# Kernel optimization log

Hardware: AMD Instinct MI355X
Metric: run time of the kernel (lower is better)

Reference implementation:

```python
import jax, jax.numpy as jnp
import numpy as np

EPS = 1e-12  # torch F.normalize eps

def _l2norm(v, axis):
    n = jnp.sqrt(jnp.sum(v * v, axis=axis, keepdims=True))
    return v / jnp.maximum(n, EPS)

def setup_inputs() -> dict:
    key = jax.random.key(0)
    k1, k2, k3 = jax.random.split(key, 3)
    N, D, H, W, K = 32, 512, 56, 56, 64
    x = jax.random.normal(k1, (N, D, H, W), dtype=jnp.float32)
    conv_w = jax.random.normal(k2, (K, D), dtype=jnp.float32) * 0.05
    centroids = jax.random.uniform(k3, (K, D), dtype=jnp.float32)
    return {"x": x, "conv_w": conv_w, "centroids": centroids}

def reference(x, conv_w, centroids):
    N, D, H, W = x.shape
    K = centroids.shape[0]
    # descriptor-wise L2 normalization over channel dim
    x = _l2norm(x, axis=1)
    x_flat = x.reshape(N, D, H * W)                      # (N, D, P)
    # 1x1 conv == per-pixel linear map: (K,D) x (N,D,P) -> (N,K,P)
    logits = jnp.einsum('kd,ndp->nkp', conv_w, x_flat)
    soft_assign = jax.nn.softmax(logits, axis=1)         # softmax over clusters
    # vlad[n,k,:] = sum_p a[n,k,p] * (x[n,:,p] - c[k,:])
    #            = (a @ x^T)[n,k,:] - (sum_p a[n,k,p]) * c[k,:]
    agg = jnp.einsum('nkp,ndp->nkd', soft_assign, x_flat)           # (N, K, D)
    a_sum = jnp.sum(soft_assign, axis=2)                            # (N, K)
    vlad = agg - a_sum[:, :, None] * centroids[None, :, :]
    vlad = _l2norm(vlad, axis=2)        # intra-normalization per cluster
    vlad = vlad.reshape(N, K * D)
    vlad = _l2norm(vlad, axis=1)        # global L2 normalization
    return vlad
```

## Files before the change

### kernel.cpp

```cpp
#include <hip/hip_runtime.h>
#include <hip/hip_bf16.h>

typedef unsigned short u16;
typedef unsigned int u32;
typedef __bf16 bf16x8 __attribute__((ext_vector_type(8)));
typedef float f32x4 __attribute__((ext_vector_type(4)));

#define N_ 32
#define D_ 512
#define P_ 3136
#define K_ 64
#define TILES_P 49
#define NDP (D_ * P_)


__device__ __forceinline__ u16 f2bf(float f) {
  u32 u = __float_as_uint(f);
  return (u16)((u + 0x7fffu + ((u >> 16) & 1u)) >> 16);
}
__device__ __forceinline__ u32 pack2(float a, float b) {
  return (u32)f2bf(a) | ((u32)f2bf(b) << 16);
}

__global__ __launch_bounds__(256) void kw_kernel(const float* __restrict__ w,
                                                 u16* __restrict__ wbf) {
  int i = blockIdx.x * 256 + threadIdx.x;
  float4 v = ((const float4*)w)[i];
  ((uint2*)wbf)[i] = make_uint2(pack2(v.x, v.y), pack2(v.z, v.w));
}

__global__ __launch_bounds__(256) void k1_kernel(const float* __restrict__ x,
                                                 const u16* __restrict__ wbf,
                                                 u16* __restrict__ a_ws,
                                                 float* __restrict__ a_sum) {
  __shared__ float a_stage[64][65];
  __shared__ float invn_s[64];

  const int t = threadIdx.x;
  const int bid = blockIdx.x;
  const int n = bid / TILES_P;
  const int tile = bid - n * TILES_P;
  const int p0 = tile * 64;
  const int lane = t & 63;
  const int w = t >> 6;
  const int c = lane & 15;
  const int q = lane >> 4;
  const int rp = w * 16 + c;

  const float* xl = x + (size_t)n * NDP + p0 + rp + (size_t)(q * 8) * P_;

  f32x4 acc[4];
#pragma unroll
  for (int m = 0; m < 4; ++m) acc[m] = (f32x4){0.f, 0.f, 0.f, 0.f};
  float sumsq = 0.f;

  float v[8];
#pragma unroll
  for (int j = 0; j < 8; ++j) v[j] = xl[j * P_];

  for (int s = 0; s < 16; ++s) {
    float vn[8];
    if (s < 15) {
      const float* xs = xl + (size_t)((s + 1) * 32) * P_;
#pragma unroll
      for (int j = 0; j < 8; ++j) vn[j] = xs[j * P_];
    }
    bf16x8 bfrag;
#pragma unroll
    for (int j = 0; j < 8; ++j) {
      sumsq += v[j] * v[j];
      bfrag[j] = (__bf16)v[j];
    }
#pragma unroll
    for (int m = 0; m < 4; ++m) {
      bf16x8 afrag = ((const bf16x8*)wbf)[(m * 16 + c) * 64 + s * 4 + q];
      acc[m] = __builtin_amdgcn_mfma_f32_16x16x32_bf16(afrag, bfrag, acc[m], 0, 0, 0);
    }
    if (s < 15) {
#pragma unroll
      for (int j = 0; j < 8; ++j) v[j] = vn[j];
    }
  }

  sumsq += __shfl_xor(sumsq, 16);
  sumsq += __shfl_xor(sumsq, 32);
  const float inv_p = 1.f / fmaxf(sqrtf(sumsq), 1e-12f);
  if (q == 0) invn_s[rp] = inv_p;

  float sc[4][4];
  float lmax = -3.0e38f;
#pragma unroll
  for (int m = 0; m < 4; ++m)
#pragma unroll
    for (int r = 0; r < 4; ++r) {
      float val = acc[m][r] * inv_p;
      sc[m][r] = val;
      lmax = fmaxf(lmax, val);
    }
  lmax = fmaxf(lmax, __shfl_xor(lmax, 16));
  lmax = fmaxf(lmax, __shfl_xor(lmax, 32));
  float lsum = 0.f;
#pragma unroll
  for (int m = 0; m < 4; ++m)
#pragma unroll
    for (int r = 0; r < 4; ++r) {
      float e = __expf(sc[m][r] - lmax);
      sc[m][r] = e;
      lsum += e;
    }
  lsum += __shfl_xor(lsum, 16);
  lsum += __shfl_xor(lsum, 32);
  const float rs = 1.f / lsum;
#pragma unroll
  for (int m = 0; m < 4; ++m)
#pragma unroll
    for (int r = 0; r < 4; ++r)
      a_stage[m * 16 + q * 4 + r][rp] = sc[m][r] * rs;
  __syncthreads();

  {
    const int k = t >> 2, pc = t & 3;
    float ssum = 0.f;
    u32 u[8];
#pragma unroll
    for (int jj = 0; jj < 8; ++jj) {
      int p = pc * 16 + jj * 2;
      float a0 = a_stage[k][p], a1 = a_stage[k][p + 1];
      ssum += a0 + a1;
      u[jj] = (u32)f2bf(a0 * invn_s[p]) | ((u32)f2bf(a1 * invn_s[p + 1]) << 16);
    }
    u16* dst = a_ws + (size_t)n * (K_ * P_) + k * P_ + p0 + pc * 16;
    ((uint4*)dst)[0] = make_uint4(u[0], u[1], u[2], u[3]);
    ((uint4*)dst)[1] = make_uint4(u[4], u[5], u[6], u[7]);
    ssum += __shfl_xor(ssum, 1);
    ssum += __shfl_xor(ssum, 2);
    if ((t & 3) == 0) atomicAdd(&a_sum[n * 64 + k], ssum);
  }
}

__global__ __launch_bounds__(256) void k2_kernel(const float* __restrict__ x,
                                                 const u16* __restrict__ a_ws,
                                                 float* __restrict__ agg) {
  const int bid = blockIdx.x;
  const int n = bid / 56;
  const int rem = bid - n * 56;
  const int dblk = rem / 7;
  const int pp = rem - dblk * 7;
  const int t = threadIdx.x;
  const int lane = t & 63, w = t >> 6;
  const int c = lane & 15, q = lane >> 4;
  const int d0 = dblk * 64 + w * 16;

  f32x4 acc[4];
#pragma unroll
  for (int m = 0; m < 4; ++m) acc[m] = (f32x4){0.f, 0.f, 0.f, 0.f};

  const bf16x8* arow = (const bf16x8*)(a_ws + (size_t)n * (K_ * P_));
  const float4* xf = (const float4*)(x + ((size_t)n * D_ + d0 + c) * P_);
  const int it0 = pp * 14, it1 = it0 + 14;

  float4 b0 = xf[it0 * 8 + q * 2];
  float4 b1 = xf[it0 * 8 + q * 2 + 1];
  bf16x8 af0 = arow[(0 * 16 + c) * 392 + it0 * 4 + q];
  bf16x8 af1 = arow[(1 * 16 + c) * 392 + it0 * 4 + q];
  bf16x8 af2 = arow[(2 * 16 + c) * 392 + it0 * 4 + q];
  bf16x8 af3 = arow[(3 * 16 + c) * 392 + it0 * 4 + q];

#pragma unroll
  for (int it = it0; it < it1; ++it) {
    float4 nb0, nb1;
    bf16x8 nf0, nf1, nf2, nf3;
    if (it + 1 < it1) {
      nb0 = xf[(it + 1) * 8 + q * 2];
      nb1 = xf[(it + 1) * 8 + q * 2 + 1];
      nf0 = arow[(0 * 16 + c) * 392 + (it + 1) * 4 + q];
      nf1 = arow[(1 * 16 + c) * 392 + (it + 1) * 4 + q];
      nf2 = arow[(2 * 16 + c) * 392 + (it + 1) * 4 + q];
      nf3 = arow[(3 * 16 + c) * 392 + (it + 1) * 4 + q];
    }
    bf16x8 bfrag;
    bfrag[0] = (__bf16)b0.x; bfrag[1] = (__bf16)b0.y;
    bfrag[2] = (__bf16)b0.z; bfrag[3] = (__bf16)b0.w;
    bfrag[4] = (__bf16)b1.x; bfrag[5] = (__bf16)b1.y;
    bfrag[6] = (__bf16)b1.z; bfrag[7] = (__bf16)b1.w;
    acc[0] = __builtin_amdgcn_mfma_f32_16x16x32_bf16(af0, bfrag, acc[0], 0, 0, 0);
    acc[1] = __builtin_amdgcn_mfma_f32_16x16x32_bf16(af1, bfrag, acc[1], 0, 0, 0);
    acc[2] = __builtin_amdgcn_mfma_f32_16x16x32_bf16(af2, bfrag, acc[2], 0, 0, 0);
    acc[3] = __builtin_amdgcn_mfma_f32_16x16x32_bf16(af3, bfrag, acc[3], 0, 0, 0);
    if (it + 1 < it1) {
      b0 = nb0; b1 = nb1; af0 = nf0; af1 = nf1; af2 = nf2; af3 = nf3;
    }
  }
  float* ob = agg + ((size_t)pp * 32 + n) * (K_ * D_);
#pragma unroll
  for (int m = 0; m < 4; ++m)
#pragma unroll
    for (int r = 0; r < 4; ++r)
      ob[(m * 16 + q * 4 + r) * D_ + d0 + c] = acc[m][r];
}

__global__ __launch_bounds__(64) void k3a_kernel(const float* __restrict__ agg,
                                                 const float* __restrict__ a_sum,
                                                 const float* __restrict__ cent,
                                                 float* __restrict__ out,
                                                 float* __restrict__ rowsq) {
  const int b = blockIdx.x;
  const int n = b >> 6, k = b & 63;
  const int t = threadIdx.x;
  const float* ab = agg + ((size_t)n * 64 + k) * 512 + t * 8;
  float v[8];
#pragma unroll
  for (int j = 0; j < 8; ++j) v[j] = 0.f;
#pragma unroll
  for (int pp = 0; pp < 7; ++pp) {
    const float4* p4 = (const float4*)(ab + (size_t)pp * 32 * (K_ * D_));
    float4 r0 = p4[0], r1 = p4[1];
    v[0] += r0.x; v[1] += r0.y; v[2] += r0.z; v[3] += r0.w;
    v[4] += r1.x; v[5] += r1.y; v[6] += r1.z; v[7] += r1.w;
  }
  const float asum = a_sum[b];
  const float4* c4 = (const float4*)(cent + k * 512 + t * 8);
  float4 c0 = c4[0], c1 = c4[1];
  v[0] -= asum * c0.x; v[1] -= asum * c0.y; v[2] -= asum * c0.z; v[3] -= asum * c0.w;
  v[4] -= asum * c1.x; v[5] -= asum * c1.y; v[6] -= asum * c1.z; v[7] -= asum * c1.w;
  float ss = 0.f;
#pragma unroll
  for (int j = 0; j < 8; ++j) ss += v[j] * v[j];
  ss += __shfl_xor(ss, 1);  ss += __shfl_xor(ss, 2);  ss += __shfl_xor(ss, 4);
  ss += __shfl_xor(ss, 8);  ss += __shfl_xor(ss, 16); ss += __shfl_xor(ss, 32);
  float4* o4 = (float4*)(out + (size_t)n * 32768 + k * 512 + t * 8);
  o4[0] = make_float4(v[0], v[1], v[2], v[3]);
  o4[1] = make_float4(v[4], v[5], v[6], v[7]);
  if (t == 0) rowsq[b] = ss;
}

__global__ __launch_bounds__(256) void k3b_kernel(const float* __restrict__ rowsq,
                                                  float* __restrict__ out) {
  __shared__ float invr_s[64];
  __shared__ float gi_s;
  const int n = blockIdx.x >> 3;
  const int seg = blockIdx.x & 7;
  const int t = threadIdx.x;
  if (t < 64) {
    float r = rowsq[n * 64 + t];
    float ri = 1.f / fmaxf(sqrtf(r), 1e-12f);
    invr_s[t] = ri;
    float g = r * ri * ri;
    g += __shfl_xor(g, 1); g += __shfl_xor(g, 2); g += __shfl_xor(g, 4);
    g += __shfl_xor(g, 8); g += __shfl_xor(g, 16); g += __shfl_xor(g, 32);
    if (t == 0) gi_s = 1.f / fmaxf(sqrtf(g), 1e-12f);
  }
  __syncthreads();
  const int e0 = seg * 4096 + t * 16;
  const float sc = invr_s[e0 >> 9] * gi_s;
  float4* o4 = (float4*)(out + (size_t)n * 32768 + e0);
#pragma unroll
  for (int i = 0; i < 4; ++i) {
    float4 vv = o4[i];
    vv.x *= sc; vv.y *= sc; vv.z *= sc; vv.w *= sc;
    o4[i] = vv;
  }
}

extern "C" void kernel_launch(void* const* d_in, const int* in_sizes, int n_in,
                              void* d_out, int out_size, void* d_ws, size_t ws_size,
                              hipStream_t stream) {
  (void)in_sizes; (void)n_in; (void)out_size; (void)ws_size;
  const float* x    = (const float*)d_in[0];
  const float* cw   = (const float*)d_in[1];
  const float* cent = (const float*)d_in[2];
  float* out = (float*)d_out;
  char* ws = (char*)d_ws;
  u16*   wbf   = (u16*)(ws);
  u16*   a_ws  = (u16*)(ws + 65536);
  float* a_sum = (float*)(ws + 12910592);
  float* agg   = (float*)(ws + 12918784);
  float* rowsq = (float*)(ws + 42278912);

  hipMemsetAsync(a_sum, 0, 64 * 32 * sizeof(float), stream);
  kw_kernel<<<32, 256, 0, stream>>>(cw, wbf);
  k1_kernel<<<32 * TILES_P, 256, 0, stream>>>(x, wbf, a_ws, a_sum);
  k2_kernel<<<1792, 256, 0, stream>>>(x, a_ws, agg);
  k3a_kernel<<<2048, 64, 0, stream>>>(agg, a_sum, cent, out, rowsq);
  k3b_kernel<<<256, 256, 0, stream>>>(rowsq, out);
}
```

Before: 393.9 us.

## Stage x tile through swizzled LDS in k1, deepen k2 prefetch, remap k2 blocks

k1 now loads the x tile with coalesced float4 reads, converts it to bf16 and writes it into a 64KB XOR-swizzled LDS buffer. The MFMA B fragments are then read from LDS, replacing strided scalar global loads along the channel dimension. The per-pixel sum of squares is reduced through shared memory, and the weight fragments are double-buffered. k2 prefetches two iterations ahead and remaps block IDs so blocks on the same XCD share batch data. The cost is 64KB of LDS per block, which likely limits occupancy, plus an extra barrier.

```diff
diff --git a/kernel.cpp b/kernel.cpp
--- a/kernel.cpp
+++ b/kernel.cpp
@@ -33,59 +33,89 @@
                                                  const u16* __restrict__ wbf,
                                                  u16* __restrict__ a_ws,
                                                  float* __restrict__ a_sum) {
-  __shared__ float a_stage[64][65];
+  __shared__ __align__(16) char xbuf[65536];
+  __shared__ float red[4][64];
   __shared__ float invn_s[64];
+  u16* X = (u16*)xbuf;
+  float (*a_stage)[65] = (float (*)[65])xbuf;
 
   const int t = threadIdx.x;
+  const int lane = t & 63;
+  const int w = t >> 6;
+  const int c = lane & 15;
+  const int q = lane >> 4;
   const int bid = blockIdx.x;
   const int n = bid / TILES_P;
   const int tile = bid - n * TILES_P;
   const int p0 = tile * 64;
-  const int lane = t & 63;
-  const int w = t >> 6;
-  const int c = lane & 15;
-  const int q = lane >> 4;
   const int rp = w * 16 + c;
 
-  const float* xl = x + (size_t)n * NDP + p0 + rp + (size_t)(q * 8) * P_;
-
-  f32x4 acc[4];
-#pragma unroll
-  for (int m = 0; m < 4; ++m) acc[m] = (f32x4){0.f, 0.f, 0.f, 0.f};
-  float sumsq = 0.f;
-
-  float v[8];
-#pragma unroll
-  for (int j = 0; j < 8; ++j) v[j] = xl[j * P_];
-
-  for (int s = 0; s < 16; ++s) {
-    float vn[8];
-    if (s < 15) {
-      const float* xs = xl + (size_t)((s + 1) * 32) * P_;
-#pragma unroll
-      for (int j = 0; j < 8; ++j) vn[j] = xs[j * P_];
-    }
-    bf16x8 bfrag;
-#pragma unroll
-    for (int j = 0; j < 8; ++j) {
-      sumsq += v[j] * v[j];
-      bfrag[j] = (__bf16)v[j];
-    }
-#pragma unroll
-    for (int m = 0; m < 4; ++m) {
-      bf16x8 afrag = ((const bf16x8*)wbf)[(m * 16 + c) * 64 + s * 4 + q];
-      acc[m] = __builtin_amdgcn_mfma_f32_16x16x32_bf16(afrag, bfrag, acc[m], 0, 0, 0);
-    }
-    if (s < 15) {
-#pragma unroll
-      for (int j = 0; j < 8; ++j) v[j] = vn[j];
-    }
-  }
-
-  sumsq += __shfl_xor(sumsq, 16);
-  sumsq += __shfl_xor(sumsq, 32);
+  const float* xg = x + (size_t)n * NDP + p0 + c * 4;
+  float La[8][4][4];
+#pragma unroll
+  for (int g = 0; g < 8; ++g) {
+    const int dr = g * 64 + w * 16 + q * 4;
+#pragma unroll
+    for (int i = 0; i < 4; ++i) {
+      float4 v4 = *(const float4*)(xg + (size_t)(dr + i) * P_);
+      La[g][i][0] = v4.x; La[g][i][1] = v4.y; La[g][i][2] = v4.z; La[g][i][3] = v4.w;
+    }
+  }
+  float ss[4] = {0.f, 0.f, 0.f, 0.f};
+#pragma unroll
+  for (int g = 0; g < 8; ++g) {
+    const int dr = g * 64 + w * 16 + q * 4;
+    const int chunk = dr >> 3;
+    const int sub = (q & 1) * 8;
+#pragma unroll
+    for (int j = 0; j < 4; ++j) {
+      float v0 = La[g][0][j], v1 = La[g][1][j], v2 = La[g][2][j], v3 = La[g][3][j];
+      ss[j] += v0 * v0 + v1 * v1 + v2 * v2 + v3 * v3;
+      const int p = c * 4 + j;
+      const int byte = p * 1024 + (((chunk ^ (p & 7)) << 4) | sub);
+      *(uint2*)(xbuf + byte) = make_uint2(pack2(v0, v1), pack2(v2, v3));
+    }
+  }
+#pragma unroll
+  for (int j = 0; j < 4; ++j) {
+    ss[j] += __shfl_xor(ss[j], 16);
+    ss[j] += __shfl_xor(ss[j], 32);
+  }
+  if (q == 0) {
+#pragma unroll
+    for (int j = 0; j < 4; ++j) red[w][c * 4 + j] = ss[j];
+  }
+  __syncthreads();
+
+  const float sumsq = red[0][rp] + red[1][rp] + red[2][rp] + red[3][rp];
   const float inv_p = 1.f / fmaxf(sqrtf(sumsq), 1e-12f);
   if (q == 0) invn_s[rp] = inv_p;
+
+  f32x4 acc[4];
+#pragma unroll
+  for (int m = 0; m < 4; ++m) acc[m] = (f32x4){0.f, 0.f, 0.f, 0.f};
+  const int ds_base = rp * 1024;
+  const int rmask = rp & 7;
+  bf16x8 af[4];
+#pragma unroll
+  for (int m = 0; m < 4; ++m) af[m] = ((const bf16x8*)wbf)[(m * 16 + c) * 64 + q];
+#pragma unroll
+  for (int s = 0; s < 16; ++s) {
+    bf16x8 afn[4];
+    if (s < 15) {
+#pragma unroll
+      for (int m = 0; m < 4; ++m)
+        afn[m] = ((const bf16x8*)wbf)[(m * 16 + c) * 64 + (s + 1) * 4 + q];
+    }
+    bf16x8 bfrag = *(const bf16x8*)(xbuf + ds_base + (((s * 4 + q) ^ rmask) << 4));
+#pragma unroll
+    for (int m = 0; m < 4; ++m)
+      acc[m] = __builtin_amdgcn_mfma_f32_16x16x32_bf16(af[m], bfrag, acc[m], 0, 0, 0);
+    if (s < 15) {
+#pragma unroll
+      for (int m = 0; m < 4; ++m) af[m] = afn[m];
+    }
+  }
 
   float sc[4][4];
   float lmax = -3.0e38f;
@@ -111,6 +141,8 @@
   lsum += __shfl_xor(lsum, 16);
   lsum += __shfl_xor(lsum, 32);
   const float rs = 1.f / lsum;
+
+  __syncthreads();
 #pragma unroll
   for (int m = 0; m < 4; ++m)
 #pragma unroll
@@ -141,7 +173,8 @@
 __global__ __launch_bounds__(256) void k2_kernel(const float* __restrict__ x,
                                                  const u16* __restrict__ a_ws,
                                                  float* __restrict__ agg) {
-  const int bid = blockIdx.x;
+  int bid = blockIdx.x;
+  bid = (bid & 7) * 224 + (bid >> 3);
   const int n = bid / 56;
   const int rem = bid - n * 56;
   const int dblk = rem / 7;
@@ -157,39 +190,39 @@
 
   const bf16x8* arow = (const bf16x8*)(a_ws + (size_t)n * (K_ * P_));
   const float4* xf = (const float4*)(x + ((size_t)n * D_ + d0 + c) * P_);
-  const int it0 = pp * 14, it1 = it0 + 14;
-
-  float4 b0 = xf[it0 * 8 + q * 2];
-  float4 b1 = xf[it0 * 8 + q * 2 + 1];
-  bf16x8 af0 = arow[(0 * 16 + c) * 392 + it0 * 4 + q];
-  bf16x8 af1 = arow[(1 * 16 + c) * 392 + it0 * 4 + q];
-  bf16x8 af2 = arow[(2 * 16 + c) * 392 + it0 * 4 + q];
-  bf16x8 af3 = arow[(3 * 16 + c) * 392 + it0 * 4 + q];
-
-#pragma unroll
-  for (int it = it0; it < it1; ++it) {
-    float4 nb0, nb1;
-    bf16x8 nf0, nf1, nf2, nf3;
-    if (it + 1 < it1) {
-      nb0 = xf[(it + 1) * 8 + q * 2];
-      nb1 = xf[(it + 1) * 8 + q * 2 + 1];
-      nf0 = arow[(0 * 16 + c) * 392 + (it + 1) * 4 + q];
-      nf1 = arow[(1 * 16 + c) * 392 + (it + 1) * 4 + q];
-      nf2 = arow[(2 * 16 + c) * 392 + (it + 1) * 4 + q];
-      nf3 = arow[(3 * 16 + c) * 392 + (it + 1) * 4 + q];
+  const int it0 = pp * 14;
+
+  float4 pb[2][2];
+  bf16x8 pa[2][4];
+#pragma unroll
+  for (int k2 = 0; k2 < 2; ++k2) {
+    pb[k2][0] = xf[(it0 + k2) * 8 + q * 2];
+    pb[k2][1] = xf[(it0 + k2) * 8 + q * 2 + 1];
+#pragma unroll
+    for (int m = 0; m < 4; ++m)
+      pa[k2][m] = arow[(m * 16 + c) * 392 + (it0 + k2) * 4 + q];
+  }
+#pragma unroll
+  for (int ii = 0; ii < 14; ++ii) {
+    const int cur = ii & 1;
+    float4 b0 = pb[cur][0], b1 = pb[cur][1];
+    bf16x8 a0_ = pa[cur][0], a1_ = pa[cur][1], a2_ = pa[cur][2], a3_ = pa[cur][3];
+    if (ii < 12) {
+      pb[cur][0] = xf[(it0 + ii + 2) * 8 + q * 2];
+      pb[cur][1] = xf[(it0 + ii + 2) * 8 + q * 2 + 1];
+#pragma unroll
+      for (int m = 0; m < 4; ++m)
+        pa[cur][m] = arow[(m * 16 + c) * 392 + (it0 + ii + 2) * 4 + q];
     }
     bf16x8 bfrag;
     bfrag[0] = (__bf16)b0.x; bfrag[1] = (__bf16)b0.y;
     bfrag[2] = (__bf16)b0.z; bfrag[3] = (__bf16)b0.w;
     bfrag[4] = (__bf16)b1.x; bfrag[5] = (__bf16)b1.y;
     bfrag[6] = (__bf16)b1.z; bfrag[7] = (__bf16)b1.w;
-    acc[0] = __builtin_amdgcn_mfma_f32_16x16x32_bf16(af0, bfrag, acc[0], 0, 0, 0);
-    acc[1] = __builtin_amdgcn_mfma_f32_16x16x32_bf16(af1, bfrag, acc[1], 0, 0, 0);
-    acc[2] = __builtin_amdgcn_mfma_f32_16x16x32_bf16(af2, bfrag, acc[2], 0, 0, 0);
-    acc[3] = __builtin_amdgcn_mfma_f32_16x16x32_bf16(af3, bfrag, acc[3], 0, 0, 0);
-    if (it + 1 < it1) {
-      b0 = nb0; b1 = nb1; af0 = nf0; af1 = nf1; af2 = nf2; af3 = nf3;
-    }
+    acc[0] = __builtin_amdgcn_mfma_f32_16x16x32_bf16(a0_, bfrag, acc[0], 0, 0, 0);
+    acc[1] = __builtin_amdgcn_mfma_f32_16x16x32_bf16(a1_, bfrag, acc[1], 0, 0, 0);
+    acc[2] = __builtin_amdgcn_mfma_f32_16x16x32_bf16(a2_, bfrag, acc[2], 0, 0, 0);
+    acc[3] = __builtin_amdgcn_mfma_f32_16x16x32_bf16(a3_, bfrag, acc[3], 0, 0, 0);
   }
   float* ob = agg + ((size_t)pp * 32 + n) * (K_ * D_);
 #pragma unroll
@@ -223,15 +256,15 @@
   float4 c0 = c4[0], c1 = c4[1];
   v[0] -= asum * c0.x; v[1] -= asum * c0.y; v[2] -= asum * c0.z; v[3] -= asum * c0.w;
   v[4] -= asum * c1.x; v[5] -= asum * c1.y; v[6] -= asum * c1.z; v[7] -= asum * c1.w;
-  float ss = 0.f;
-#pragma unroll
-  for (int j = 0; j < 8; ++j) ss += v[j] * v[j];
-  ss += __shfl_xor(ss, 1);  ss += __shfl_xor(ss, 2);  ss += __shfl_xor(ss, 4);
-  ss += __shfl_xor(ss, 8);  ss += __shfl_xor(ss, 16); ss += __shfl_xor(ss, 32);
+  float ssq = 0.f;
+#pragma unroll
+  for (int j = 0; j < 8; ++j) ssq += v[j] * v[j];
+  ssq += __shfl_xor(ssq, 1);  ssq += __shfl_xor(ssq, 2);  ssq += __shfl_xor(ssq, 4);
+  ssq += __shfl_xor(ssq, 8);  ssq += __shfl_xor(ssq, 16); ssq += __shfl_xor(ssq, 32);
   float4* o4 = (float4*)(out + (size_t)n * 32768 + k * 512 + t * 8);
   o4[0] = make_float4(v[0], v[1], v[2], v[3]);
   o4[1] = make_float4(v[4], v[5], v[6], v[7]);
-  if (t == 0) rowsq[b] = ss;
+  if (t == 0) rowsq[b] = ssq;
 }
 
 __global__ __launch_bounds__(256) void k3b_kernel(const float* __restrict__ rowsq,
```

New measurement: 403.2 us. 1.02x slower.

## Pre-convert x to bf16 and transpose it for the logits GEMM

Applied to the files above, without the earlier changes.

Adds a pass that casts the whole input to bf16. A second pass transposes it to pixel-major layout and precomputes per-pixel squared norms. The logits kernel then loads contiguous bf16x8 fragments with two-deep prefetch, and the aggregation kernel reads bf16 x instead of fp32. The aggregation grid ordering is remapped, and the residual kernel packs four clusters per 256-thread block. In exchange, the extra cast and transpose passes add substantial memory traffic. The transpose uses scalar strided 16-bit loads, and the norms are now computed from bf16-rounded values.

```diff
diff --git a/kernel.cpp b/kernel.cpp
--- a/kernel.cpp
+++ b/kernel.cpp
@@ -29,13 +29,61 @@
   ((uint2*)wbf)[i] = make_uint2(pack2(v.x, v.y), pack2(v.z, v.w));
 }
 
-__global__ __launch_bounds__(256) void k1_kernel(const float* __restrict__ x,
+__global__ __launch_bounds__(256) void tbf_kernel(const float* __restrict__ x,
+                                                  u16* __restrict__ xbf) {
+  const int nf4 = (N_ * NDP) / 4;
+  for (int i = blockIdx.x * 256 + threadIdx.x; i < nf4; i += 2048 * 256) {
+    float4 v = ((const float4*)x)[i];
+    ((uint2*)xbf)[i] = make_uint2(pack2(v.x, v.y), pack2(v.z, v.w));
+  }
+}
+
+__global__ __launch_bounds__(256) void tt_kernel(const u16* __restrict__ xbf,
+                                                 u16* __restrict__ xt,
+                                                 float* __restrict__ psum) {
+  const int bid = blockIdx.x;
+  const int n = bid / TILES_P;
+  const int tile = bid - n * TILES_P;
+  const int p0 = tile * 64;
+  const int t = threadIdx.x;
+  const int lane = t & 63;
+  const int w = t >> 6;
+  const int c = lane & 15;
+  const int q = lane >> 4;
+  const int gpx = p0 + w * 16 + c;
+
+  const u16* src = xbf + (size_t)n * NDP + gpx;
+  u16* dst = xt + ((size_t)n * P_ + gpx) * D_;
+  float s0 = 0.f, s1 = 0.f;
+#pragma unroll
+  for (int it = 0; it < 16; ++it) {
+    const u16* sp = src + (size_t)(it * 32 + q * 8) * P_;
+    u32 u[4];
+#pragma unroll
+    for (int j = 0; j < 4; ++j) {
+      u32 lo = sp[(size_t)(2 * j) * P_];
+      u32 hi = sp[(size_t)(2 * j + 1) * P_];
+      u[j] = lo | (hi << 16);
+      float f0 = __uint_as_float(lo << 16);
+      float f1 = __uint_as_float(hi << 16);
+      s0 += f0 * f0;
+      s1 += f1 * f1;
+    }
+    *(uint4*)(dst + it * 32 + q * 8) = make_uint4(u[0], u[1], u[2], u[3]);
+  }
+  float ssq = s0 + s1;
+  ssq += __shfl_xor(ssq, 16);
+  ssq += __shfl_xor(ssq, 32);
+  if (q == 0) psum[n * P_ + gpx] = ssq;
+}
+
+__global__ __launch_bounds__(256) void k1_kernel(const u16* __restrict__ xt,
                                                  const u16* __restrict__ wbf,
+                                                 const float* __restrict__ psum,
                                                  u16* __restrict__ a_ws,
                                                  float* __restrict__ a_sum) {
   __shared__ float a_stage[64][65];
   __shared__ float invn_s[64];
-
   const int t = threadIdx.x;
   const int bid = blockIdx.x;
   const int n = bid / TILES_P;
@@ -47,45 +95,42 @@
   const int q = lane >> 4;
   const int rp = w * 16 + c;
 
-  const float* xl = x + (size_t)n * NDP + p0 + rp + (size_t)(q * 8) * P_;
+  if (t < 64)
+    invn_s[t] = 1.f / fmaxf(sqrtf(psum[n * P_ + p0 + t]), 1e-12f);
+  const float inv_p = 1.f / fmaxf(sqrtf(psum[n * P_ + p0 + rp]), 1e-12f);
+
+  const bf16x8* brow = (const bf16x8*)(xt + ((size_t)n * P_ + p0 + rp) * D_);
+  const bf16x8* wrow = (const bf16x8*)wbf;
 
   f32x4 acc[4];
 #pragma unroll
   for (int m = 0; m < 4; ++m) acc[m] = (f32x4){0.f, 0.f, 0.f, 0.f};
-  float sumsq = 0.f;
-
-  float v[8];
-#pragma unroll
-  for (int j = 0; j < 8; ++j) v[j] = xl[j * P_];
-
+
+  bf16x8 pb[2];
+  bf16x8 pa[2][4];
+  pb[0] = brow[q];
+  pb[1] = brow[4 + q];
+#pragma unroll
+  for (int m = 0; m < 4; ++m) {
+    pa[0][m] = wrow[(m * 16 + c) * 64 + q];
+    pa[1][m] = wrow[(m * 16 + c) * 64 + 4 + q];
+  }
+#pragma unroll
   for (int s = 0; s < 16; ++s) {
-    float vn[8];
-    if (s < 15) {
-      const float* xs = xl + (size_t)((s + 1) * 32) * P_;
-#pragma unroll
-      for (int j = 0; j < 8; ++j) vn[j] = xs[j * P_];
-    }
-    bf16x8 bfrag;
-#pragma unroll
-    for (int j = 0; j < 8; ++j) {
-      sumsq += v[j] * v[j];
-      bfrag[j] = (__bf16)v[j];
-    }
-#pragma unroll
-    for (int m = 0; m < 4; ++m) {
-      bf16x8 afrag = ((const bf16x8*)wbf)[(m * 16 + c) * 64 + s * 4 + q];
-      acc[m] = __builtin_amdgcn_mfma_f32_16x16x32_bf16(afrag, bfrag, acc[m], 0, 0, 0);
-    }
-    if (s < 15) {
-#pragma unroll
-      for (int j = 0; j < 8; ++j) v[j] = vn[j];
-    }
-  }
-
-  sumsq += __shfl_xor(sumsq, 16);
-  sumsq += __shfl_xor(sumsq, 32);
-  const float inv_p = 1.f / fmaxf(sqrtf(sumsq), 1e-12f);
-  if (q == 0) invn_s[rp] = inv_p;
+    const int cur = s & 1;
+    bf16x8 bfr = pb[cur];
+    bf16x8 a0 = pa[cur][0], a1 = pa[cur][1], a2 = pa[cur][2], a3 = pa[cur][3];
+    if (s < 14) {
+      pb[cur] = brow[(s + 2) * 4 + q];
+#pragma unroll
+      for (int m = 0; m < 4; ++m)
+        pa[cur][m] = wrow[(m * 16 + c) * 64 + (s + 2) * 4 + q];
+    }
+    acc[0] = __builtin_amdgcn_mfma_f32_16x16x32_bf16(a0, bfr, acc[0], 0, 0, 0);
+    acc[1] = __builtin_amdgcn_mfma_f32_16x16x32_bf16(a1, bfr, acc[1], 0, 0, 0);
+    acc[2] = __builtin_amdgcn_mfma_f32_16x16x32_bf16(a2, bfr, acc[2], 0, 0, 0);
+    acc[3] = __builtin_amdgcn_mfma_f32_16x16x32_bf16(a3, bfr, acc[3], 0, 0, 0);
+  }
 
   float sc[4][4];
   float lmax = -3.0e38f;
@@ -138,14 +183,14 @@
   }
 }
 
-__global__ __launch_bounds__(256) void k2_kernel(const float* __restrict__ x,
+__global__ __launch_bounds__(256) void k2_kernel(const u16* __restrict__ xbf,
                                                  const u16* __restrict__ a_ws,
                                                  float* __restrict__ agg) {
-  const int bid = blockIdx.x;
-  const int n = bid / 56;
-  const int rem = bid - n * 56;
-  const int dblk = rem / 7;
-  const int pp = rem - dblk * 7;
+  const int b = blockIdx.x;
+  const int dblk = (b >> 3) & 7;
+  const int npp = (b >> 6) * 8 + (b & 7);
+  const int n = npp / 7;
+  const int pp = npp - n * 7;
   const int t = threadIdx.x;
   const int lane = t & 63, w = t >> 6;
   const int c = lane & 15, q = lane >> 4;
@@ -155,41 +200,33 @@
 #pragma unroll
   for (int m = 0; m < 4; ++m) acc[m] = (f32x4){0.f, 0.f, 0.f, 0.f};
 
-  const bf16x8* arow = (const bf16x8*)(a_ws + (size_t)n * (K_ * P_));
-  const float4* xf = (const float4*)(x + ((size_t)n * D_ + d0 + c) * P_);
-  const int it0 = pp * 14, it1 = it0 + 14;
-
-  float4 b0 = xf[it0 * 8 + q * 2];
-  float4 b1 = xf[it0 * 8 + q * 2 + 1];
-  bf16x8 af0 = arow[(0 * 16 + c) * 392 + it0 * 4 + q];
-  bf16x8 af1 = arow[(1 * 16 + c) * 392 + it0 * 4 + q];
-  bf16x8 af2 = arow[(2 * 16 + c) * 392 + it0 * 4 + q];
-  bf16x8 af3 = arow[(3 * 16 + c) * 392 + it0 * 4 + q];
-
-#pragma unroll
-  for (int it = it0; it < it1; ++it) {
-    float4 nb0, nb1;
-    bf16x8 nf0, nf1, nf2, nf3;
-    if (it + 1 < it1) {
-      nb0 = xf[(it + 1) * 8 + q * 2];
-      nb1 = xf[(it + 1) * 8 + q * 2 + 1];
-      nf0 = arow[(0 * 16 + c) * 392 + (it + 1) * 4 + q];
-      nf1 = arow[(1 * 16 + c) * 392 + (it + 1) * 4 + q];
-      nf2 = arow[(2 * 16 + c) * 392 + (it + 1) * 4 + q];
-      nf3 = arow[(3 * 16 + c) * 392 + (it + 1) * 4 + q];
-    }
-    bf16x8 bfrag;
-    bfrag[0] = (__bf16)b0.x; bfrag[1] = (__bf16)b0.y;
-    bfrag[2] = (__bf16)b0.z; bfrag[3] = (__bf16)b0.w;
-    bfrag[4] = (__bf16)b1.x; bfrag[5] = (__bf16)b1.y;
-    bfrag[6] = (__bf16)b1.z; bfrag[7] = (__bf16)b1.w;
-    acc[0] = __builtin_amdgcn_mfma_f32_16x16x32_bf16(af0, bfrag, acc[0], 0, 0, 0);
-    acc[1] = __builtin_amdgcn_mfma_f32_16x16x32_bf16(af1, bfrag, acc[1], 0, 0, 0);
-    acc[2] = __builtin_amdgcn_mfma_f32_16x16x32_bf16(af2, bfrag, acc[2], 0, 0, 0);
-    acc[3] = __builtin_amdgcn_mfma_f32_16x16x32_bf16(af3, bfrag, acc[3], 0, 0, 0);
-    if (it + 1 < it1) {
-      b0 = nb0; b1 = nb1; af0 = nf0; af1 = nf1; af2 = nf2; af3 = nf3;
-    }
+  const u16* ab = a_ws + (size_t)n * (K_ * P_) + pp * 448 + q * 8;
+  const u16* xb = xbf + ((size_t)n * D_ + d0 + c) * P_ + pp * 448 + q * 8;
+
+  bf16x8 pb[2];
+  bf16x8 pa[2][4];
+#pragma unroll
+  for (int k2 = 0; k2 < 2; ++k2) {
+    pb[k2] = *(const bf16x8*)(xb + k2 * 32);
+#pragma unroll
+    for (int m = 0; m < 4; ++m)
+      pa[k2][m] = *(const bf16x8*)(ab + (size_t)(m * 16 + c) * P_ + k2 * 32);
+  }
+#pragma unroll
+  for (int it = 0; it < 14; ++it) {
+    const int cur = it & 1;
+    bf16x8 bfr = pb[cur];
+    bf16x8 a0 = pa[cur][0], a1 = pa[cur][1], a2 = pa[cur][2], a3 = pa[cur][3];
+    if (it < 12) {
+      pb[cur] = *(const bf16x8*)(xb + (it + 2) * 32);
+#pragma unroll
+      for (int m = 0; m < 4; ++m)
+        pa[cur][m] = *(const bf16x8*)(ab + (size_t)(m * 16 + c) * P_ + (it + 2) * 32);
+    }
+    acc[0] = __builtin_amdgcn_mfma_f32_16x16x32_bf16(a0, bfr, acc[0], 0, 0, 0);
+    acc[1] = __builtin_amdgcn_mfma_f32_16x16x32_bf16(a1, bfr, acc[1], 0, 0, 0);
+    acc[2] = __builtin_amdgcn_mfma_f32_16x16x32_bf16(a2, bfr, acc[2], 0, 0, 0);
+    acc[3] = __builtin_amdgcn_mfma_f32_16x16x32_bf16(a3, bfr, acc[3], 0, 0, 0);
   }
   float* ob = agg + ((size_t)pp * 32 + n) * (K_ * D_);
 #pragma unroll
@@ -199,15 +236,17 @@
       ob[(m * 16 + q * 4 + r) * D_ + d0 + c] = acc[m][r];
 }
 
-__global__ __launch_bounds__(64) void k3a_kernel(const float* __restrict__ agg,
-                                                 const float* __restrict__ a_sum,
-                                                 const float* __restrict__ cent,
-                                                 float* __restrict__ out,
-                                                 float* __restrict__ rowsq) {
+__global__ __launch_bounds__(256) void k3a_kernel(const float* __restrict__ agg,
+                                                  const float* __restrict__ a_sum,
+                                                  const float* __restrict__ cent,
+                                                  float* __restrict__ out,
+                                                  float* __restrict__ rowsq) {
   const int b = blockIdx.x;
-  const int n = b >> 6, k = b & 63;
-  const int t = threadIdx.x;
-  const float* ab = agg + ((size_t)n * 64 + k) * 512 + t * 8;
+  const int n = b >> 4, kg = b & 15;
+  const int t = threadIdx.x;
+  const int lane = t & 63, w = t >> 6;
+  const int k = kg * 4 + w;
+  const float* ab = agg + ((size_t)n * 64 + k) * 512 + lane * 8;
   float v[8];
 #pragma unroll
   for (int j = 0; j < 8; ++j) v[j] = 0.f;
@@ -218,20 +257,20 @@
     v[0] += r0.x; v[1] += r0.y; v[2] += r0.z; v[3] += r0.w;
     v[4] += r1.x; v[5] += r1.y; v[6] += r1.z; v[7] += r1.w;
   }
-  const float asum = a_sum[b];
-  const float4* c4 = (const float4*)(cent + k * 512 + t * 8);
+  const float asum = a_sum[n * 64 + k];
+  const float4* c4 = (const float4*)(cent + k * 512 + lane * 8);
   float4 c0 = c4[0], c1 = c4[1];
   v[0] -= asum * c0.x; v[1] -= asum * c0.y; v[2] -= asum * c0.z; v[3] -= asum * c0.w;
   v[4] -= asum * c1.x; v[5] -= asum * c1.y; v[6] -= asum * c1.z; v[7] -= asum * c1.w;
-  float ss = 0.f;
-#pragma unroll
-  for (int j = 0; j < 8; ++j) ss += v[j] * v[j];
-  ss += __shfl_xor(ss, 1);  ss += __shfl_xor(ss, 2);  ss += __shfl_xor(ss, 4);
-  ss += __shfl_xor(ss, 8);  ss += __shfl_xor(ss, 16); ss += __shfl_xor(ss, 32);
-  float4* o4 = (float4*)(out + (size_t)n * 32768 + k * 512 + t * 8);
+  float ssq = 0.f;
+#pragma unroll
+  for (int j = 0; j < 8; ++j) ssq += v[j] * v[j];
+  ssq += __shfl_xor(ssq, 1);  ssq += __shfl_xor(ssq, 2);  ssq += __shfl_xor(ssq, 4);
+  ssq += __shfl_xor(ssq, 8);  ssq += __shfl_xor(ssq, 16); ssq += __shfl_xor(ssq, 32);
+  float4* o4 = (float4*)(out + (size_t)n * 32768 + k * 512 + lane * 8);
   o4[0] = make_float4(v[0], v[1], v[2], v[3]);
   o4[1] = make_float4(v[4], v[5], v[6], v[7]);
-  if (t == 0) rowsq[b] = ss;
+  if (lane == 0) rowsq[n * 64 + k] = ssq;
 }
 
 __global__ __launch_bounds__(256) void k3b_kernel(const float* __restrict__ rowsq,
@@ -276,11 +315,16 @@
   float* a_sum = (float*)(ws + 12910592);
   float* agg   = (float*)(ws + 12918784);
   float* rowsq = (float*)(ws + 42278912);
+  u16*   xbf   = (u16*)(ws + 42287104);
+  u16*   x_t   = (u16*)(ws + 145047552);
+  float* psum  = (float*)(ws + 247808000);
 
   hipMemsetAsync(a_sum, 0, 64 * 32 * sizeof(float), stream);
   kw_kernel<<<32, 256, 0, stream>>>(cw, wbf);
-  k1_kernel<<<32 * TILES_P, 256, 0, stream>>>(x, wbf, a_ws, a_sum);
-  k2_kernel<<<1792, 256, 0, stream>>>(x, a_ws, agg);
-  k3a_kernel<<<2048, 64, 0, stream>>>(agg, a_sum, cent, out, rowsq);
+  tbf_kernel<<<2048, 256, 0, stream>>>(x, xbf);
+  tt_kernel<<<32 * TILES_P, 256, 0, stream>>>(xbf, x_t, psum);
+  k1_kernel<<<32 * TILES_P, 256, 0, stream>>>(x_t, wbf, psum, a_ws, a_sum);
+  k2_kernel<<<1792, 256, 0, stream>>>(xbf, a_ws, agg);
+  k3a_kernel<<<512, 256, 0, stream>>>(agg, a_sum, cent, out, rowsq);
   k3b_kernel<<<256, 256, 0, stream>>>(rowsq, out);
 }
```

Result: slower. 491.7 us (+24.8%).

## Fuse soft-assignment and aggregation into one LDS-staged kernel reading x once

Applied to the files above, without the earlier changes.

Merges the logits/softmax kernel and the aggregation GEMM into a single kernel. Each block owns one batch item and a range of pixel tiles, stages a 512x64 fp32 x tile into 128KB of LDS with a swizzle via global_load_lds, and computes both GEMMs from that shared copy. The aim is to read x from HBM once instead of twice and to skip the bf16 assignment round-trip through global memory. In exchange only 256 blocks of one wave-group each run, with 128 fp32 accumulators per thread and no overlap between loads and compute, so latency hiding and occupancy may suffer.

```diff
diff --git a/kernel.cpp b/kernel.cpp
--- a/kernel.cpp
+++ b/kernel.cpp
@@ -10,7 +10,6 @@
 #define D_ 512
 #define P_ 3136
 #define K_ 64
-#define TILES_P 49
 #define NDP (D_ * P_)
 
 
@@ -29,209 +28,232 @@
   ((uint2*)wbf)[i] = make_uint2(pack2(v.x, v.y), pack2(v.z, v.w));
 }
 
-__global__ __launch_bounds__(256) void k1_kernel(const float* __restrict__ x,
-                                                 const u16* __restrict__ wbf,
-                                                 u16* __restrict__ a_ws,
-                                                 float* __restrict__ a_sum) {
+__global__ __launch_bounds__(256, 1) void f_kernel(const float* __restrict__ x,
+                                                   const u16* __restrict__ wbf,
+                                                   float* __restrict__ agg,
+                                                   float* __restrict__ a_sum) {
+  __shared__ __align__(16) char xbuf[131072];
   __shared__ float a_stage[64][65];
   __shared__ float invn_s[64];
+  __shared__ __align__(16) char a_bf[8192];
 
   const int t = threadIdx.x;
-  const int bid = blockIdx.x;
-  const int n = bid / TILES_P;
-  const int tile = bid - n * TILES_P;
-  const int p0 = tile * 64;
   const int lane = t & 63;
   const int w = t >> 6;
   const int c = lane & 15;
   const int q = lane >> 4;
+  const int b = blockIdx.x;
+  const int n = b >> 3;
+  const int s = b & 7;
+  const int tile0 = (s == 0) ? 0 : 7 + (s - 1) * 6;
+  const int ntl = (s == 0) ? 7 : 6;
   const int rp = w * 16 + c;
-
-  const float* xl = x + (size_t)n * NDP + p0 + rp + (size_t)(q * 8) * P_;
-
-  f32x4 acc[4];
-#pragma unroll
-  for (int m = 0; m < 4; ++m) acc[m] = (f32x4){0.f, 0.f, 0.f, 0.f};
-  float sumsq = 0.f;
-
-  float v[8];
-#pragma unroll
-  for (int j = 0; j < 8; ++j) v[j] = xl[j * P_];
-
-  for (int s = 0; s < 16; ++s) {
-    float vn[8];
-    if (s < 15) {
-      const float* xs = xl + (size_t)((s + 1) * 32) * P_;
-#pragma unroll
-      for (int j = 0; j < 8; ++j) vn[j] = xs[j * P_];
-    }
-    bf16x8 bfrag;
-#pragma unroll
-    for (int j = 0; j < 8; ++j) {
-      sumsq += v[j] * v[j];
-      bfrag[j] = (__bf16)v[j];
-    }
+  const int rpc = rp >> 2;
+  const int rpo = (rp & 3) * 4;
+  const int c7 = c & 7;
+
+  const bf16x8* wrow = (const bf16x8*)wbf;
+  const char* xgb = (const char*)(x + (size_t)n * NDP);
+
+  f32x4 acc2[4][8];
+#pragma unroll
+  for (int m = 0; m < 4; ++m)
+#pragma unroll
+    for (int i = 0; i < 8; ++i) acc2[m][i] = (f32x4){0.f, 0.f, 0.f, 0.f};
+  float ssum_acc = 0.f;
+
+  for (int tt = 0; tt < ntl; ++tt) {
+    const int p0 = (tile0 + tt) * 64;
+
+#pragma unroll
+    for (int i = 0; i < 32; ++i) {
+      const int d = w * 128 + i * 4 + q;
+      const char* src = xgb + ((size_t)d * P_ + p0) * 4 + ((c ^ (d & 7)) << 4);
+      __builtin_amdgcn_global_load_lds(
+          (const __attribute__((address_space(1))) void*)src,
+          (__attribute__((address_space(3))) void*)(xbuf + w * 32768 + i * 1024),
+          16, 0, 0);
+    }
+    __syncthreads();
+
+    f32x4 acc[4];
+#pragma unroll
+    for (int m = 0; m < 4; ++m) acc[m] = (f32x4){0.f, 0.f, 0.f, 0.f};
+    float sumsq = 0.f;
+    bf16x8 pa[2][4];
 #pragma unroll
     for (int m = 0; m < 4; ++m) {
-      bf16x8 afrag = ((const bf16x8*)wbf)[(m * 16 + c) * 64 + s * 4 + q];
-      acc[m] = __builtin_amdgcn_mfma_f32_16x16x32_bf16(afrag, bfrag, acc[m], 0, 0, 0);
-    }
-    if (s < 15) {
-#pragma unroll
-      for (int j = 0; j < 8; ++j) v[j] = vn[j];
-    }
+      pa[0][m] = wrow[(m * 16 + c) * 64 + q];
+      pa[1][m] = wrow[(m * 16 + c) * 64 + 4 + q];
+    }
+    float vc[8];
+#pragma unroll
+    for (int j = 0; j < 8; ++j)
+      vc[j] = *(const float*)(xbuf + ((q * 8 + j) << 8) + ((rpc ^ j) << 4) + rpo);
+#pragma unroll
+    for (int st = 0; st < 16; ++st) {
+      float vn[8];
+      if (st < 15) {
+#pragma unroll
+        for (int j = 0; j < 8; ++j)
+          vn[j] = *(const float*)(xbuf + (((st + 1) * 32 + q * 8 + j) << 8) +
+                                  ((rpc ^ j) << 4) + rpo);
+      }
+      bf16x8 bfr;
+#pragma unroll
+      for (int j = 0; j < 8; ++j) {
+        sumsq += vc[j] * vc[j];
+        bfr[j] = (__bf16)vc[j];
+      }
+      bf16x8 nf[4];
+      if (st < 14) {
+#pragma unroll
+        for (int m = 0; m < 4; ++m)
+          nf[m] = wrow[(m * 16 + c) * 64 + (st + 2) * 4 + q];
+      }
+#pragma unroll
+      for (int m = 0; m < 4; ++m)
+        acc[m] = __builtin_amdgcn_mfma_f32_16x16x32_bf16(pa[st & 1][m], bfr, acc[m], 0, 0, 0);
+      if (st < 14) {
+#pragma unroll
+        for (int m = 0; m < 4; ++m) pa[st & 1][m] = nf[m];
+      }
+      if (st < 15) {
+#pragma unroll
+        for (int j = 0; j < 8; ++j) vc[j] = vn[j];
+      }
+    }
+
+    sumsq += __shfl_xor(sumsq, 16);
+    sumsq += __shfl_xor(sumsq, 32);
+    const float inv_p = 1.f / fmaxf(sqrtf(sumsq), 1e-12f);
+    if (q == 0) invn_s[rp] = inv_p;
+
+    float sc[4][4];
+    float lmax = -3.0e38f;
+#pragma unroll
+    for (int m = 0; m < 4; ++m)
+#pragma unroll
+      for (int r = 0; r < 4; ++r) {
+        float val = acc[m][r] * inv_p;
+        sc[m][r] = val;
+        lmax = fmaxf(lmax, val);
+      }
+    lmax = fmaxf(lmax, __shfl_xor(lmax, 16));
+    lmax = fmaxf(lmax, __shfl_xor(lmax, 32));
+    float lsum = 0.f;
+#pragma unroll
+    for (int m = 0; m < 4; ++m)
+#pragma unroll
+      for (int r = 0; r < 4; ++r) {
+        float e = __expf(sc[m][r] - lmax);
+        sc[m][r] = e;
+        lsum += e;
+      }
+    lsum += __shfl_xor(lsum, 16);
+    lsum += __shfl_xor(lsum, 32);
+    const float rs = 1.f / lsum;
+#pragma unroll
+    for (int m = 0; m < 4; ++m)
+#pragma unroll
+      for (int r = 0; r < 4; ++r)
+        a_stage[m * 16 + q * 4 + r][rp] = sc[m][r] * rs;
+    __syncthreads();
+
+    {
+      const int k = t >> 2, pc4 = t & 3;
+      float ssum = 0.f;
+      u32 u[8];
+#pragma unroll
+      for (int jj = 0; jj < 8; ++jj) {
+        int p = pc4 * 16 + jj * 2;
+        float a0 = a_stage[k][p], a1 = a_stage[k][p + 1];
+        ssum += a0 + a1;
+        u[jj] = (u32)f2bf(a0 * invn_s[p]) | ((u32)f2bf(a1 * invn_s[p + 1]) << 16);
+      }
+      *(uint4*)(a_bf + k * 128 + (((pc4 * 2) ^ (k & 7)) << 4)) =
+          make_uint4(u[0], u[1], u[2], u[3]);
+      *(uint4*)(a_bf + k * 128 + (((pc4 * 2 + 1) ^ (k & 7)) << 4)) =
+          make_uint4(u[4], u[5], u[6], u[7]);
+      ssum_acc += ssum;
+    }
+    __syncthreads();
+
+#pragma unroll
+    for (int st = 0; st < 2; ++st) {
+      bf16x8 afr[4];
+#pragma unroll
+      for (int m = 0; m < 4; ++m)
+        afr[m] = *(const bf16x8*)(a_bf + (m * 16 + c) * 128 +
+                                  (((st * 4 + q) ^ c7) << 4));
+      const int pc0 = st * 8 + q * 2;
+#pragma unroll
+      for (int nt = 0; nt < 8; ++nt) {
+        const int d = w * 128 + nt * 16 + c;
+        f32x4 b0 = *(const f32x4*)(xbuf + (d << 8) + ((pc0 ^ c7) << 4));
+        f32x4 b1 = *(const f32x4*)(xbuf + (d << 8) + (((pc0 + 1) ^ c7) << 4));
+        bf16x8 bfr;
+#pragma unroll
+        for (int i4 = 0; i4 < 4; ++i4) {
+          bfr[i4] = (__bf16)b0[i4];
+          bfr[4 + i4] = (__bf16)b1[i4];
+        }
+#pragma unroll
+        for (int m = 0; m < 4; ++m)
+          acc2[m][nt] = __builtin_amdgcn_mfma_f32_16x16x32_bf16(afr[m], bfr, acc2[m][nt], 0, 0, 0);
+      }
+    }
+    __syncthreads();
   }
 
-  sumsq += __shfl_xor(sumsq, 16);
-  sumsq += __shfl_xor(sumsq, 32);
-  const float inv_p = 1.f / fmaxf(sqrtf(sumsq), 1e-12f);
-  if (q == 0) invn_s[rp] = inv_p;
-
-  float sc[4][4];
-  float lmax = -3.0e38f;
+  float* ob = agg + ((size_t)s * 32 + n) * (K_ * D_);
 #pragma unroll
   for (int m = 0; m < 4; ++m)
 #pragma unroll
-    for (int r = 0; r < 4; ++r) {
-      float val = acc[m][r] * inv_p;
-      sc[m][r] = val;
-      lmax = fmaxf(lmax, val);
-    }
-  lmax = fmaxf(lmax, __shfl_xor(lmax, 16));
-  lmax = fmaxf(lmax, __shfl_xor(lmax, 32));
-  float lsum = 0.f;
-#pragma unroll
-  for (int m = 0; m < 4; ++m)
-#pragma unroll
-    for (int r = 0; r < 4; ++r) {
-      float e = __expf(sc[m][r] - lmax);
-      sc[m][r] = e;
-      lsum += e;
-    }
-  lsum += __shfl_xor(lsum, 16);
-  lsum += __shfl_xor(lsum, 32);
-  const float rs = 1.f / lsum;
-#pragma unroll
-  for (int m = 0; m < 4; ++m)
-#pragma unroll
-    for (int r = 0; r < 4; ++r)
-      a_stage[m * 16 + q * 4 + r][rp] = sc[m][r] * rs;
-  __syncthreads();
-
-  {
-    const int k = t >> 2, pc = t & 3;
-    float ssum = 0.f;
-    u32 u[8];
-#pragma unroll
-    for (int jj = 0; jj < 8; ++jj) {
-      int p = pc * 16 + jj * 2;
-      float a0 = a_stage[k][p], a1 = a_stage[k][p + 1];
-      ssum += a0 + a1;
-      u[jj] = (u32)f2bf(a0 * invn_s[p]) | ((u32)f2bf(a1 * invn_s[p + 1]) << 16);
-    }
-    u16* dst = a_ws + (size_t)n * (K_ * P_) + k * P_ + p0 + pc * 16;
-    ((uint4*)dst)[0] = make_uint4(u[0], u[1], u[2], u[3]);
-    ((uint4*)dst)[1] = make_uint4(u[4], u[5], u[6], u[7]);
-    ssum += __shfl_xor(ssum, 1);
-    ssum += __shfl_xor(ssum, 2);
-    if ((t & 3) == 0) atomicAdd(&a_sum[n * 64 + k], ssum);
-  }
-}
-
-__global__ __launch_bounds__(256) void k2_kernel(const float* __restrict__ x,
-                                                 const u16* __restrict__ a_ws,
-                                                 float* __restrict__ agg) {
-  const int bid = blockIdx.x;
-  const int n = bid / 56;
-  const int rem = bid - n * 56;
-  const int dblk = rem / 7;
-  const int pp = rem - dblk * 7;
+    for (int nt = 0; nt < 8; ++nt)
+#pragma unroll
+      for (int r = 0; r < 4; ++r)
+        ob[(m * 16 + q * 4 + r) * D_ + w * 128 + nt * 16 + c] = acc2[m][nt][r];
+  ssum_acc += __shfl_xor(ssum_acc, 1);
+  ssum_acc += __shfl_xor(ssum_acc, 2);
+  if ((t & 3) == 0) atomicAdd(&a_sum[n * 64 + (t >> 2)], ssum_acc);
+}
+
+__global__ __launch_bounds__(256) void k3a_kernel(const float* __restrict__ agg,
+                                                  const float* __restrict__ a_sum,
+                                                  const float* __restrict__ cent,
+                                                  float* __restrict__ out,
+                                                  float* __restrict__ rowsq) {
+  const int b = blockIdx.x;
+  const int n = b >> 4, kg = b & 15;
   const int t = threadIdx.x;
   const int lane = t & 63, w = t >> 6;
-  const int c = lane & 15, q = lane >> 4;
-  const int d0 = dblk * 64 + w * 16;
-
-  f32x4 acc[4];
-#pragma unroll
-  for (int m = 0; m < 4; ++m) acc[m] = (f32x4){0.f, 0.f, 0.f, 0.f};
-
-  const bf16x8* arow = (const bf16x8*)(a_ws + (size_t)n * (K_ * P_));
-  const float4* xf = (const float4*)(x + ((size_t)n * D_ + d0 + c) * P_);
-  const int it0 = pp * 14, it1 = it0 + 14;
-
-  float4 b0 = xf[it0 * 8 + q * 2];
-  float4 b1 = xf[it0 * 8 + q * 2 + 1];
-  bf16x8 af0 = arow[(0 * 16 + c) * 392 + it0 * 4 + q];
-  bf16x8 af1 = arow[(1 * 16 + c) * 392 + it0 * 4 + q];
-  bf16x8 af2 = arow[(2 * 16 + c) * 392 + it0 * 4 + q];
-  bf16x8 af3 = arow[(3 * 16 + c) * 392 + it0 * 4 + q];
-
-#pragma unroll
-  for (int it = it0; it < it1; ++it) {
-    float4 nb0, nb1;
-    bf16x8 nf0, nf1, nf2, nf3;
-    if (it + 1 < it1) {
-      nb0 = xf[(it + 1) * 8 + q * 2];
-      nb1 = xf[(it + 1) * 8 + q * 2 + 1];
-      nf0 = arow[(0 * 16 + c) * 392 + (it + 1) * 4 + q];
-      nf1 = arow[(1 * 16 + c) * 392 + (it + 1) * 4 + q];
-      nf2 = arow[(2 * 16 + c) * 392 + (it + 1) * 4 + q];
-      nf3 = arow[(3 * 16 + c) * 392 + (it + 1) * 4 + q];
-    }
-    bf16x8 bfrag;
-    bfrag[0] = (__bf16)b0.x; bfrag[1] = (__bf16)b0.y;
-    bfrag[2] = (__bf16)b0.z; bfrag[3] = (__bf16)b0.w;
-    bfrag[4] = (__bf16)b1.x; bfrag[5] = (__bf16)b1.y;
-    bfrag[6] = (__bf16)b1.z; bfrag[7] = (__bf16)b1.w;
-    acc[0] = __builtin_amdgcn_mfma_f32_16x16x32_bf16(af0, bfrag, acc[0], 0, 0, 0);
-    acc[1] = __builtin_amdgcn_mfma_f32_16x16x32_bf16(af1, bfrag, acc[1], 0, 0, 0);
-    acc[2] = __builtin_amdgcn_mfma_f32_16x16x32_bf16(af2, bfrag, acc[2], 0, 0, 0);
-    acc[3] = __builtin_amdgcn_mfma_f32_16x16x32_bf16(af3, bfrag, acc[3], 0, 0, 0);
-    if (it + 1 < it1) {
-      b0 = nb0; b1 = nb1; af0 = nf0; af1 = nf1; af2 = nf2; af3 = nf3;
-    }
-  }
-  float* ob = agg + ((size_t)pp * 32 + n) * (K_ * D_);
-#pragma unroll
-  for (int m = 0; m < 4; ++m)
-#pragma unroll
-    for (int r = 0; r < 4; ++r)
-      ob[(m * 16 + q * 4 + r) * D_ + d0 + c] = acc[m][r];
-}
-
-__global__ __launch_bounds__(64) void k3a_kernel(const float* __restrict__ agg,
-                                                 const float* __restrict__ a_sum,
-                                                 const float* __restrict__ cent,
-                                                 float* __restrict__ out,
-                                                 float* __restrict__ rowsq) {
-  const int b = blockIdx.x;
-  const int n = b >> 6, k = b & 63;
-  const int t = threadIdx.x;
-  const float* ab = agg + ((size_t)n * 64 + k) * 512 + t * 8;
+  const int k = kg * 4 + w;
+  const float* ab = agg + ((size_t)n * 64 + k) * 512 + lane * 8;
   float v[8];
 #pragma unroll
   for (int j = 0; j < 8; ++j) v[j] = 0.f;
 #pragma unroll
-  for (int pp = 0; pp < 7; ++pp) {
+  for (int pp = 0; pp < 8; ++pp) {
     const float4* p4 = (const float4*)(ab + (size_t)pp * 32 * (K_ * D_));
     float4 r0 = p4[0], r1 = p4[1];
     v[0] += r0.x; v[1] += r0.y; v[2] += r0.z; v[3] += r0.w;
     v[4] += r1.x; v[5] += r1.y; v[6] += r1.z; v[7] += r1.w;
   }
-  const float asum = a_sum[b];
-  const float4* c4 = (const float4*)(cent + k * 512 + t * 8);
+  const float asum = a_sum[n * 64 + k];
+  const float4* c4 = (const float4*)(cent + k * 512 + lane * 8);
   float4 c0 = c4[0], c1 = c4[1];
   v[0] -= asum * c0.x; v[1] -= asum * c0.y; v[2] -= asum * c0.z; v[3] -= asum * c0.w;
   v[4] -= asum * c1.x; v[5] -= asum * c1.y; v[6] -= asum * c1.z; v[7] -= asum * c1.w;
-  float ss = 0.f;
-#pragma unroll
-  for (int j = 0; j < 8; ++j) ss += v[j] * v[j];
-  ss += __shfl_xor(ss, 1);  ss += __shfl_xor(ss, 2);  ss += __shfl_xor(ss, 4);
-  ss += __shfl_xor(ss, 8);  ss += __shfl_xor(ss, 16); ss += __shfl_xor(ss, 32);
-  float4* o4 = (float4*)(out + (size_t)n * 32768 + k * 512 + t * 8);
+  float ssq = 0.f;
+#pragma unroll
+  for (int j = 0; j < 8; ++j) ssq += v[j] * v[j];
+  ssq += __shfl_xor(ssq, 1);  ssq += __shfl_xor(ssq, 2);  ssq += __shfl_xor(ssq, 4);
+  ssq += __shfl_xor(ssq, 8);  ssq += __shfl_xor(ssq, 16); ssq += __shfl_xor(ssq, 32);
+  float4* o4 = (float4*)(out + (size_t)n * 32768 + k * 512 + lane * 8);
   o4[0] = make_float4(v[0], v[1], v[2], v[3]);
   o4[1] = make_float4(v[4], v[5], v[6], v[7]);
-  if (t == 0) rowsq[b] = ss;
+  if (lane == 0) rowsq[n * 64 + k] = ssq;
 }
 
 __global__ __launch_bounds__(256) void k3b_kernel(const float* __restrict__ rowsq,
@@ -272,15 +294,13 @@
   float* out = (float*)d_out;
   char* ws = (char*)d_ws;
   u16*   wbf   = (u16*)(ws);
-  u16*   a_ws  = (u16*)(ws + 65536);
-  float* a_sum = (float*)(ws + 12910592);
-  float* agg   = (float*)(ws + 12918784);
-  float* rowsq = (float*)(ws + 42278912);
+  float* a_sum = (float*)(ws + 65536);
+  float* agg   = (float*)(ws + 73728);
+  float* rowsq = (float*)(ws + 33628160);
 
   hipMemsetAsync(a_sum, 0, 64 * 32 * sizeof(float), stream);
   kw_kernel<<<32, 256, 0, stream>>>(cw, wbf);
-  k1_kernel<<<32 * TILES_P, 256, 0, stream>>>(x, wbf, a_ws, a_sum);
-  k2_kernel<<<1792, 256, 0, stream>>>(x, a_ws, agg);
-  k3a_kernel<<<2048, 64, 0, stream>>>(agg, a_sum, cent, out, rowsq);
+  f_kernel<<<256, 256, 0, stream>>>(x, wbf, agg, a_sum);
+  k3a_kernel<<<512, 256, 0, stream>>>(agg, a_sum, cent, out, rowsq);
   k3b_kernel<<<256, 256, 0, stream>>>(rowsq, out);
 }
```

New measurement: 368.4 us. 1.07x faster.
